# Optimization experiments

Hardware: AMD Instinct MI355X
Metric: run time of the kernel (lower is better)

The kernel has to match this reference:

```python
import jax, jax.numpy as jnp
import numpy as np

GROUP = 128  # K-rows per scale group, matching (in_features+127)//128 scale rows


def setup_inputs() -> dict:
    key = jax.random.key(0)
    k1, k2, k3, k4, k5, k6 = jax.random.split(key, 6)
    M, K, N = 512, 8192, 8192
    x = jax.random.normal(k1, (M, K), dtype=jnp.float32)
    # packed 4-bit codes: each byte holds two nibble indices along N -> [K, N//2]
    packed = jax.random.randint(k2, (K, N // 2), 0, 256, dtype=jnp.int32)
    grid = jax.random.normal(k3, (16,), dtype=jnp.float32)  # 2^bits codebook entries
    scales = jax.random.uniform(k4, (K // GROUP, N), dtype=jnp.float32)
    su = jax.random.normal(k5, (K,), dtype=jnp.float32)
    sv = jax.random.normal(k6, (N,), dtype=jnp.float32)
    return {"x": x, "packed": packed, "grid": grid, "scales": scales, "su": su, "sv": sv}


def _dequant(packed, grid, scales, su, sv):
    # Unpack two 4-bit indices per byte (low nibble first) along N.
    K = packed.shape[0]
    N = packed.shape[1] * 2
    low = packed & 0xF
    high = (packed >> 4) & 0xF
    idx = jnp.stack([low, high], axis=-1).reshape(K, N)  # [K, N] codes in [0,16)
    w = grid[idx]                                        # codebook lookup
    # per-group (128 K-rows) x per-output-column scales
    w = (w.reshape(K // GROUP, GROUP, N) * scales[:, None, :]).reshape(K, N)
    # input/output sign/scale vectors
    return w * su[:, None] * sv[None, :]


def reference(x, packed, grid, scales, su, sv):
    W = _dequant(packed, grid, scales, su, sv)  # [K, N]
    return x @ W                                 # [M, N]
```

## Files before the change

kernel.cpp:

```cpp
#include <hip/hip_runtime.h>


typedef __attribute__((ext_vector_type(8))) short short8;
typedef __attribute__((ext_vector_type(4))) float f32x4;

__device__ __forceinline__ unsigned short f2bf(float f) {
  unsigned int u = __builtin_bit_cast(unsigned int, f);
  u += 0x7FFFu + ((u >> 16) & 1u);
  return (unsigned short)(u >> 16);
}

__device__ __forceinline__ void gld16(const void* g, void* l) {
  __builtin_amdgcn_global_load_lds(
      (__attribute__((address_space(1))) void*)(g),
      (__attribute__((address_space(3))) void*)(l), 16, 0, 0);
}

__global__ __launch_bounds__(256) void zero_out(float4* __restrict__ p, int n4) {
  int i = blockIdx.x * 256 + threadIdx.x;
  int stride = gridDim.x * 256;
  for (; i < n4; i += stride) p[i] = float4{0.f, 0.f, 0.f, 0.f};
}

__global__ __launch_bounds__(256) void convert_x_su(
    const float* __restrict__ x, const float* __restrict__ su,
    unsigned short* __restrict__ xp, int K) {
  int k = blockIdx.x * 2048 + threadIdx.x * 8;
  size_t i = (size_t)blockIdx.y * K + k;
  float4 x0 = *(const float4*)(x + i);
  float4 x1 = *(const float4*)(x + i + 4);
  float4 s0 = *(const float4*)(su + k);
  float4 s1 = *(const float4*)(su + k + 4);
  unsigned int r0 = f2bf(x0.x * s0.x) | ((unsigned int)f2bf(x0.y * s0.y) << 16);
  unsigned int r1 = f2bf(x0.z * s0.z) | ((unsigned int)f2bf(x0.w * s0.w) << 16);
  unsigned int r2 = f2bf(x1.x * s1.x) | ((unsigned int)f2bf(x1.y * s1.y) << 16);
  unsigned int r3 = f2bf(x1.z * s1.z) | ((unsigned int)f2bf(x1.w * s1.w) << 16);
  uint4 o; o.x = r0; o.y = r1; o.z = r2; o.w = r3;
  *(uint4*)(xp + i) = o;
}

#define BM 128
#define BN 128
#define BK 64
#define KSLICES 4

__global__ __launch_bounds__(256, 3) void gemm_fused(
    const unsigned short* __restrict__ A,
    const int* __restrict__ packed,
    const float* __restrict__ gridv,
    const float* __restrict__ scales,
    const float* __restrict__ sv,
    float* __restrict__ C, int M, int N, int K) {
  __shared__ unsigned short As[BM * BK];
  __shared__ unsigned short Bs[BN * BK];
  __shared__ float sS[16 * 128];
  __shared__ float sGp[32];

  int t = threadIdx.x;
  int l = t & 63;
  int w = t >> 6;

  int nwg = gridDim.x;
  int bid = blockIdx.x;
  int swz = (bid & 7) * (nwg >> 3) + (bid >> 3);
  int mblocks = M >> 7;
  int mb = swz % mblocks;
  int nb = swz / mblocks;
  size_t m0 = (size_t)mb * BM;
  size_t n0 = (size_t)nb * BN;
  int kbeg = blockIdx.y * (K / KSLICES);
  int kend = kbeg + K / KSLICES;

  if (t < 16) { float g = gridv[t]; sGp[t * 2] = g; sGp[t * 2 + 1] = g; }
  int g0 = kbeg >> 7;
  for (int i = t; i < 16 * 128; i += 256) {
    int g = i >> 7, n = i & 127;
    sS[i] = scales[(size_t)(g0 + g) * N + n0 + n] * sv[n0 + n];
  }
  __syncthreads();

  const unsigned short* Ag = A + m0 * K;
  size_t rs = (size_t)(N >> 1);
  int c = l;
  int kq = w;
  const int* pbase = packed + (n0 >> 1) + c + (size_t)(kq * 16) * rs;
  const float* lut = &sGp[l & 1];

  int srow = t >> 3, sch = t & 7;
  int lr = l & 15, lh = l >> 4;
  int wr = w >> 1, wc = w & 1;
  int nA = 2 * c, nB = 2 * c + 1;

  f32x4 acc[4][4] = {};

  int pv[16];
  {
    const int* p = pbase + (size_t)kbeg * rs;
#pragma unroll
    for (int j = 0; j < 16; ++j) pv[j] = p[(size_t)j * rs];
  }

  for (int k0 = kbeg; k0 < kend; k0 += BK) {
    int gl = (k0 - kbeg) >> 7;
    float2 a2 = *(const float2*)&sS[gl * 128 + nA];
#pragma unroll
    for (int q = 0; q < 2; ++q) {
      int ch = kq * 2 + q;
      uint4 va, vb;
      unsigned int* pa = (unsigned int*)&va;
      unsigned int* pbv = (unsigned int*)&vb;
#pragma unroll
      for (int d = 0; d < 4; ++d) {
        int v0 = pv[q * 8 + 2 * d], v1 = pv[q * 8 + 2 * d + 1];
        float w00 = lut[(v0 & 15) << 1];
        float w01 = lut[(v1 & 15) << 1];
        float w10 = lut[((v0 >> 4) & 15) << 1];
        float w11 = lut[((v1 >> 4) & 15) << 1];
        pa[d]  = (unsigned int)f2bf(w00 * a2.x) | ((unsigned int)f2bf(w01 * a2.x) << 16);
        pbv[d] = (unsigned int)f2bf(w10 * a2.y) | ((unsigned int)f2bf(w11 * a2.y) << 16);
      }
      *(uint4*)&Bs[nA * BK + ((ch ^ (nA & 7)) << 3)] = va;
      *(uint4*)&Bs[nB * BK + ((ch ^ (nB & 7)) << 3)] = vb;
    }

#pragma unroll
    for (int r = 0; r < 4; ++r) {
      int row = r * 32 + srow;
      int sc = (sch ^ (row & 7)) * 8;
      gld16(Ag + (size_t)row * K + k0 + sc, &As[row * BK + sch * 8]);
    }
    __syncthreads();

    int pvn[16] = {};
    if (k0 + BK < kend) {
      const int* p = pbase + (size_t)(k0 + BK) * rs;
#pragma unroll
      for (int j = 0; j < 16; ++j) pvn[j] = p[(size_t)j * rs];
    }

#pragma unroll
    for (int kh = 0; kh < 2; ++kh) {
      short8 a[4], b[4];
      int sk = kh * 4 + lh;
#pragma unroll
      for (int i = 0; i < 4; ++i) {
        int row = wr * 64 + i * 16 + lr;
        a[i] = *(const short8*)&As[row * BK + ((sk ^ (row & 7)) << 3)];
      }
#pragma unroll
      for (int j = 0; j < 4; ++j) {
        int row = wc * 64 + j * 16 + lr;
        b[j] = *(const short8*)&Bs[row * BK + ((sk ^ (row & 7)) << 3)];
      }
#pragma unroll
      for (int i = 0; i < 4; ++i)
#pragma unroll
        for (int j = 0; j < 4; ++j)
          acc[i][j] = __builtin_amdgcn_mfma_f32_16x16x32_bf16(a[i], b[j], acc[i][j], 0, 0, 0);
    }
    __syncthreads();

#pragma unroll
    for (int j = 0; j < 16; ++j) pv[j] = pvn[j];
  }

#pragma unroll
  for (int i = 0; i < 4; ++i)
#pragma unroll
    for (int j = 0; j < 4; ++j) {
      size_t row = m0 + wr * 64 + i * 16 + lh * 4;
      size_t col = n0 + wc * 64 + j * 16 + lr;
#pragma unroll
      for (int r = 0; r < 4; ++r)
        atomicAdd(&C[(row + r) * N + col], acc[i][j][r]);
    }
}

extern "C" void kernel_launch(void* const* d_in, const int* in_sizes, int n_in,
                              void* d_out, int out_size, void* d_ws, size_t ws_size,
                              hipStream_t stream) {
  const float* x      = (const float*)d_in[0];
  const int*   packed = (const int*)d_in[1];
  const float* gridv  = (const float*)d_in[2];
  const float* scales = (const float*)d_in[3];
  const float* su     = (const float*)d_in[4];
  const float* sv     = (const float*)d_in[5];
  float* out = (float*)d_out;

  int K = in_sizes[4];
  int N = in_sizes[5];
  int M = in_sizes[0] / K;

  unsigned short* xp = (unsigned short*)d_ws;

  zero_out<<<1024, 256, 0, stream>>>((float4*)out, (M * N) / 4);
  convert_x_su<<<dim3(K / 2048, M), 256, 0, stream>>>(x, su, xp, K);
  int nwg = (N / BN) * (M / BM);
  gemm_fused<<<dim3(nwg, KSLICES), 256, 0, stream>>>(xp, packed, gridv, scales, sv,
                                                     out, M, N, K);
}
```

Baseline: 326.9 us.

## Double-buffer LDS and software-pipeline dequant with 256x64x32 tiles

```diff
diff --git a/kernel.cpp b/kernel.cpp
--- a/kernel.cpp
+++ b/kernel.cpp
@@ -39,10 +39,10 @@
   *(uint4*)(xp + i) = o;
 }
 
-#define BM 128
-#define BN 128
-#define BK 64
-#define KSLICES 4
+#define BM 256
+#define BN 64
+#define BK 32
+#define KS 4
 
 __global__ __launch_bounds__(256, 3) void gemm_fused(
     const unsigned short* __restrict__ A,
@@ -51,10 +51,10 @@
     const float* __restrict__ scales,
     const float* __restrict__ sv,
     float* __restrict__ C, int M, int N, int K) {
-  __shared__ unsigned short As[BM * BK];
-  __shared__ unsigned short Bs[BN * BK];
-  __shared__ float sS[16 * 128];
-  __shared__ float sGp[32];
+  __shared__ unsigned short As[2][BM * BK];
+  __shared__ unsigned short Bs[2][BN * BK];
+  __shared__ float sS[16 * BN];
+  __shared__ float sGd[32];
 
   int t = threadIdx.x;
   int l = t & 63;
@@ -63,113 +63,119 @@
   int nwg = gridDim.x;
   int bid = blockIdx.x;
   int swz = (bid & 7) * (nwg >> 3) + (bid >> 3);
-  int mblocks = M >> 7;
-  int mb = swz % mblocks;
-  int nb = swz / mblocks;
+  int mbs = M / BM;
+  int mb = swz % mbs;
+  int nb = swz / mbs;
   size_t m0 = (size_t)mb * BM;
   size_t n0 = (size_t)nb * BN;
-  int kbeg = blockIdx.y * (K / KSLICES);
-  int kend = kbeg + K / KSLICES;
-
-  if (t < 16) { float g = gridv[t]; sGp[t * 2] = g; sGp[t * 2 + 1] = g; }
+  int kbeg = blockIdx.y * (K / KS);
+  const int NT = (K / KS) / BK;
+
+  if (t < 16) { float g = gridv[t]; sGd[2 * t] = g; sGd[2 * t + 1] = g; }
   int g0 = kbeg >> 7;
-  for (int i = t; i < 16 * 128; i += 256) {
-    int g = i >> 7, n = i & 127;
+  for (int i = t; i < 16 * BN; i += 256) {
+    int g = i >> 6, n = i & 63;
     sS[i] = scales[(size_t)(g0 + g) * N + n0 + n] * sv[n0 + n];
   }
   __syncthreads();
 
   const unsigned short* Ag = A + m0 * K;
+  int arow = l >> 2;
+  int asrc_ch = (l & 3) ^ ((l >> 3) & 3);
+#define STAGE_A(BUF, K0)                                                    \
+  {                                                                         \
+    _Pragma("unroll") for (int r_ = 0; r_ < 4; ++r_) {                      \
+      int gi_ = w * 4 + r_;                                                 \
+      int row_ = gi_ * 16 + arow;                                           \
+      gld16(Ag + (size_t)row_ * K + (K0) + asrc_ch * 8,                     \
+            &As[BUF][gi_ * 512 + l * 8]);                                   \
+    }                                                                       \
+  }
+
   size_t rs = (size_t)(N >> 1);
-  int c = l;
-  int kq = w;
-  const int* pbase = packed + (n0 >> 1) + c + (size_t)(kq * 16) * rs;
-  const float* lut = &sGp[l & 1];
-
-  int srow = t >> 3, sch = t & 7;
+  const int* pb = packed + (n0 >> 1) + (l >> 1) + (size_t)(w * 8) * rs;
+#define LOAD_CODES(PV, TT)                                                  \
+  {                                                                         \
+    const int* p_ = pb + (size_t)(kbeg + (TT) * BK) * rs;                   \
+    _Pragma("unroll") for (int j_ = 0; j_ < 8; ++j_)                        \
+        PV[j_] = p_[(size_t)j_ * rs];                                       \
+  }
+
+  int par = l & 1;
+  int nsh = par * 4;
+  int bw_ch = (w ^ ((l >> 1) & 3)) * 8;
+#define DEQUANT(PV, BUF, GRP)                                               \
+  {                                                                         \
+    float an_ = sS[(GRP) * BN + l];                                         \
+    unsigned int u_[4];                                                     \
+    _Pragma("unroll") for (int q_ = 0; q_ < 4; ++q_) {                      \
+      int nib0_ = (PV[2 * q_] >> nsh) & 15;                                 \
+      int nib1_ = (PV[2 * q_ + 1] >> nsh) & 15;                             \
+      float f0_ = sGd[nib0_ * 2 + par] * an_;                               \
+      float f1_ = sGd[nib1_ * 2 + par] * an_;                               \
+      asm("v_cvt_pk_bf16_f32 %0, %1, %2" : "=v"(u_[q_]) : "v"(f0_), "v"(f1_)); \
+    }                                                                       \
+    uint4 vv_; vv_.x = u_[0]; vv_.y = u_[1]; vv_.z = u_[2]; vv_.w = u_[3];  \
+    *(uint4*)&Bs[BUF][l * BK + bw_ch] = vv_;                                \
+  }
+
   int lr = l & 15, lh = l >> 4;
-  int wr = w >> 1, wc = w & 1;
-  int nA = 2 * c, nB = 2 * c + 1;
-
+  int fr_ch = (lh ^ ((lr >> 1) & 3)) << 3;
   f32x4 acc[4][4] = {};
-
-  int pv[16];
-  {
-    const int* p = pbase + (size_t)kbeg * rs;
-#pragma unroll
-    for (int j = 0; j < 16; ++j) pv[j] = p[(size_t)j * rs];
-  }
-
-  for (int k0 = kbeg; k0 < kend; k0 += BK) {
-    int gl = (k0 - kbeg) >> 7;
-    float2 a2 = *(const float2*)&sS[gl * 128 + nA];
-#pragma unroll
-    for (int q = 0; q < 2; ++q) {
-      int ch = kq * 2 + q;
-      uint4 va, vb;
-      unsigned int* pa = (unsigned int*)&va;
-      unsigned int* pbv = (unsigned int*)&vb;
-#pragma unroll
-      for (int d = 0; d < 4; ++d) {
-        int v0 = pv[q * 8 + 2 * d], v1 = pv[q * 8 + 2 * d + 1];
-        float w00 = lut[(v0 & 15) << 1];
-        float w01 = lut[(v1 & 15) << 1];
-        float w10 = lut[((v0 >> 4) & 15) << 1];
-        float w11 = lut[((v1 >> 4) & 15) << 1];
-        pa[d]  = (unsigned int)f2bf(w00 * a2.x) | ((unsigned int)f2bf(w01 * a2.x) << 16);
-        pbv[d] = (unsigned int)f2bf(w10 * a2.y) | ((unsigned int)f2bf(w11 * a2.y) << 16);
-      }
-      *(uint4*)&Bs[nA * BK + ((ch ^ (nA & 7)) << 3)] = va;
-      *(uint4*)&Bs[nB * BK + ((ch ^ (nB & 7)) << 3)] = vb;
-    }
-
-#pragma unroll
-    for (int r = 0; r < 4; ++r) {
-      int row = r * 32 + srow;
-      int sc = (sch ^ (row & 7)) * 8;
-      gld16(Ag + (size_t)row * K + k0 + sc, &As[row * BK + sch * 8]);
-    }
-    __syncthreads();
-
-    int pvn[16] = {};
-    if (k0 + BK < kend) {
-      const int* p = pbase + (size_t)(k0 + BK) * rs;
-#pragma unroll
-      for (int j = 0; j < 16; ++j) pvn[j] = p[(size_t)j * rs];
-    }
-
-#pragma unroll
-    for (int kh = 0; kh < 2; ++kh) {
-      short8 a[4], b[4];
-      int sk = kh * 4 + lh;
-#pragma unroll
-      for (int i = 0; i < 4; ++i) {
-        int row = wr * 64 + i * 16 + lr;
-        a[i] = *(const short8*)&As[row * BK + ((sk ^ (row & 7)) << 3)];
-      }
-#pragma unroll
-      for (int j = 0; j < 4; ++j) {
-        int row = wc * 64 + j * 16 + lr;
-        b[j] = *(const short8*)&Bs[row * BK + ((sk ^ (row & 7)) << 3)];
-      }
-#pragma unroll
-      for (int i = 0; i < 4; ++i)
-#pragma unroll
-        for (int j = 0; j < 4; ++j)
-          acc[i][j] = __builtin_amdgcn_mfma_f32_16x16x32_bf16(a[i], b[j], acc[i][j], 0, 0, 0);
-    }
-    __syncthreads();
-
-#pragma unroll
-    for (int j = 0; j < 16; ++j) pv[j] = pvn[j];
-  }
-
+#define MFMA_PHASE(BUF)                                                     \
+  {                                                                         \
+    short8 a_[4], b_[4];                                                    \
+    _Pragma("unroll") for (int i_ = 0; i_ < 4; ++i_) {                      \
+      int row_ = w * 64 + i_ * 16 + lr;                                     \
+      a_[i_] = *(const short8*)&As[BUF][row_ * BK + fr_ch];                 \
+    }                                                                       \
+    _Pragma("unroll") for (int j_ = 0; j_ < 4; ++j_) {                      \
+      int row_ = j_ * 16 + lr;                                              \
+      b_[j_] = *(const short8*)&Bs[BUF][row_ * BK + fr_ch];                 \
+    }                                                                       \
+    _Pragma("unroll") for (int i_ = 0; i_ < 4; ++i_)                        \
+        _Pragma("unroll") for (int j_ = 0; j_ < 4; ++j_)                    \
+            acc[i_][j_] = __builtin_amdgcn_mfma_f32_16x16x32_bf16(          \
+                a_[i_], b_[j_], acc[i_][j_], 0, 0, 0);                      \
+  }
+
+  int pv[8], pvn[8];
+
+  STAGE_A(0, kbeg);
+  __builtin_amdgcn_sched_barrier(0);
+  LOAD_CODES(pv, 0);
+  DEQUANT(pv, 0, 0);
+  LOAD_CODES(pv, 1);
+  asm volatile("s_waitcnt vmcnt(8) lgkmcnt(0)" ::: "memory");
+  __builtin_amdgcn_s_barrier();
+
+#define ITER(T, CUR, PV, PVN)                                               \
+  {                                                                         \
+    if ((T) + 1 < NT) {                                                     \
+      STAGE_A((CUR) ^ 1, kbeg + ((T) + 1) * BK);                            \
+      __builtin_amdgcn_sched_barrier(0);                                    \
+      int t2_ = ((T) + 2 < NT) ? (T) + 2 : NT - 1;                          \
+      LOAD_CODES(PVN, t2_);                                                 \
+      DEQUANT(PV, (CUR) ^ 1, ((T) + 1) >> 2);                               \
+    }                                                                       \
+    MFMA_PHASE(CUR);                                                        \
+    asm volatile("s_waitcnt vmcnt(8) lgkmcnt(0)" ::: "memory");             \
+    __builtin_amdgcn_s_barrier();                                           \
+  }
+
+#pragma unroll 1
+  for (int tt = 0; tt < NT; tt += 2) {
+    ITER(tt, 0, pv, pvn);
+    ITER(tt + 1, 1, pvn, pv);
+  }
+
+  int lq = l >> 4;
 #pragma unroll
   for (int i = 0; i < 4; ++i)
 #pragma unroll
     for (int j = 0; j < 4; ++j) {
-      size_t row = m0 + wr * 64 + i * 16 + lh * 4;
-      size_t col = n0 + wc * 64 + j * 16 + lr;
+      size_t row = m0 + w * 64 + i * 16 + lq * 4;
+      size_t col = n0 + j * 16 + lr;
 #pragma unroll
       for (int r = 0; r < 4; ++r)
         atomicAdd(&C[(row + r) * N + col], acc[i][j][r]);
@@ -195,7 +201,7 @@
 
   zero_out<<<1024, 256, 0, stream>>>((float4*)out, (M * N) / 4);
   convert_x_su<<<dim3(K / 2048, M), 256, 0, stream>>>(x, su, xp, K);
-  int nwg = (N / BN) * (M / BM);
-  gemm_fused<<<dim3(nwg, KSLICES), 256, 0, stream>>>(xp, packed, gridv, scales, sv,
-                                                     out, M, N, K);
-}
+  int nwg = (M / BM) * (N / BN);
+  gemm_fused<<<dim3(nwg, KS), 256, 0, stream>>>(xp, packed, gridv, scales, sv,
+                                                out, M, N, K);
+}
```

Result: slower. 363.7 us (+11.3%).
